# Kernel tuning notes

Hardware: AMD Instinct MI355X
Metric: run time of the kernel (lower is better)

The kernel has to match this reference:

```python
import jax, jax.numpy as jnp
import numpy as np
from jax import lax

DIM = 2048
HEAD_DIM = 128
N_HEADS = 16
N_KV_HEADS = 4
N_REP = N_HEADS // N_KV_HEADS
K_CHUNK = 8          # token_chunk
SEQ = 2048
BATCH = 1
ROPE_THETA = 10000.0
KV_DIM = N_KV_HEADS * HEAD_DIM  # 512


def _make_freq_cis(seq, hd, theta):
    # (seq, hd//2, 2, 2) rotation matrices [[cos, -sin], [sin, cos]]
    inv = 1.0 / (theta ** (np.arange(0, hd, 2, dtype=np.float64) / hd))
    ang = np.outer(np.arange(seq, dtype=np.float64), inv)
    cos, sin = np.cos(ang), np.sin(ang)
    f = np.stack([np.stack([cos, -sin], -1), np.stack([sin, cos], -1)], -2)
    return jnp.asarray(f, jnp.float32)


def setup_inputs() -> dict:
    key = jax.random.key(0)
    ks = jax.random.split(key, 12)
    s = 0.02
    inp = {
        'x': jax.random.normal(ks[0], (BATCH, SEQ, DIM), jnp.float32),
        'freq_cis': _make_freq_cis(SEQ, HEAD_DIM, ROPE_THETA),
        # nn.Linear weights stored as (out, in); y = x @ W.T
        'wq': jax.random.normal(ks[1], (N_HEADS * HEAD_DIM, DIM), jnp.float32) * s,
        'wk': jax.random.normal(ks[2], (KV_DIM, DIM), jnp.float32) * s,
        'wv': jax.random.normal(ks[3], (KV_DIM, DIM), jnp.float32) * s,
        'wo': jax.random.normal(ks[4], (DIM, N_HEADS * HEAD_DIM), jnp.float32) * s,
        # diagonal SSM params for k_ssm / v_ssm (per-channel)
        'a_log_k': jax.random.normal(ks[5], (KV_DIM,), jnp.float32) * 0.5,
        'b_k': jax.random.normal(ks[6], (KV_DIM,), jnp.float32),
        'c_k': jax.random.normal(ks[7], (KV_DIM,), jnp.float32),
        'a_log_v': jax.random.normal(ks[8], (KV_DIM,), jnp.float32) * 0.5,
        'b_v': jax.random.normal(ks[9], (KV_DIM,), jnp.float32),
        'c_v': jax.random.normal(ks[10], (KV_DIM,), jnp.float32),
    }
    return inp


def _ssm_chunked(x, a_log, b, c):
    # Chunked diagonal SSM with state reset every K_CHUNK tokens
    # (equivalent to flat_process_chunks_with_ssm with boundaries every K).
    bsz, S, E = x.shape
    nc = S // K_CHUNK
    a = jnp.exp(-jax.nn.softplus(a_log))  # (E,) decay in (0, 1)
    xs = x.reshape(bsz * nc, K_CHUNK, E).swapaxes(0, 1)  # (K, N, E)

    def step(h, xt):
        h = a * h + b * xt
        return h, c * h

    _, ys = lax.scan(step, jnp.zeros((bsz * nc, E), x.dtype), xs)
    return ys.swapaxes(0, 1).reshape(bsz, S, E)


def _apply_rope(xq, xk, freq_cis):
    # xq: (b, s, h, hd); freq_cis: (s, hd//2, 2, 2)
    def rot(t):
        b, s, h, hd = t.shape
        tr = t.reshape(b, s, h, hd // 2, 1, 2)
        f = freq_cis.reshape(1, s, 1, hd // 2, 2, 2)
        return (tr * f).sum(-1).reshape(b, s, h, hd)
    return rot(xq), rot(xk)


def _forward(x, freq_cis, wq, wk, wv, wo, a_log_k, b_k, c_k, a_log_v, b_v, c_v):
    bsz, S, _ = x.shape
    xq = jnp.einsum('bsd,ed->bse', x, wq)
    xk = jnp.einsum('bsd,ed->bse', x, wk)
    xv = jnp.einsum('bsd,ed->bse', x, wv)

    # chunked SSM preprocessing of K/V (+ residual_ssm)
    xk_p = _ssm_chunked(xk, a_log_k, b_k, c_k) + xk
    xv_p = _ssm_chunked(xv, a_log_v, b_v, c_v) + xv

    xq = xq.reshape(bsz, S, N_HEADS, HEAD_DIM)
    xk_p = xk_p.reshape(bsz, S, N_KV_HEADS, HEAD_DIM)
    xv_p = xv_p.reshape(bsz, S, N_KV_HEADS, HEAD_DIM)

    xq, xk_p = _apply_rope(xq, xk_p, freq_cis)

    # GQA repeat_kv (torch.repeat_interleave on head dim)
    xk_p = jnp.repeat(xk_p, N_REP, axis=2)
    xv_p = jnp.repeat(xv_p, N_REP, axis=2)

    # chunk-boundary attention mask
    k_pos = jnp.arange(S)
    boundary = (k_pos % K_CHUNK) == (K_CHUNK - 1)
    t = jnp.arange(S)[:, None]
    k = k_pos[None, :]
    mask = ((k < t) & boundary[None, :]) | (k == t - 1) | ((k < 4) & (k <= t))

    q = xq.transpose(0, 2, 1, 3)   # (b, h, s, d)
    kk = xk_p.transpose(0, 2, 1, 3)
    vv = xv_p.transpose(0, 2, 1, 3)

    scores = jnp.einsum('bhqd,bhkd->bhqk', q, kk) / jnp.sqrt(
        jnp.asarray(HEAD_DIM, q.dtype))
    scores = jnp.where(mask[None, None], scores, -jnp.inf)
    attn = jax.nn.softmax(scores, axis=-1)
    out = jnp.einsum('bhqk,bhkd->bhqd', attn, vv)
    out = out.transpose(0, 2, 1, 3).reshape(bsz, S, N_HEADS * HEAD_DIM)
    return jnp.einsum('bse,de->bsd', out, wo)


def reference(x, freq_cis, wq, wk, wv, wo, a_log_k, b_k, c_k,
              a_log_v, b_v, c_v):
    return _forward(x, freq_cis, wq, wk, wv, wo,
                    a_log_k, b_k, c_k, a_log_v, b_v, c_v)
```

## Files before the change

kernel.cpp:

```cpp
#include <hip/hip_runtime.h>

typedef __bf16 bf16x8 __attribute__((ext_vector_type(8)));
typedef float  f32x4  __attribute__((ext_vector_type(4)));
typedef unsigned short u16;
typedef unsigned int   u32;

__device__ __forceinline__ float b2f(u16 u) {
    u32 x = ((u32)u) << 16;
    return __builtin_bit_cast(float, x);
}
__device__ __forceinline__ u16 f2b(float f) {
    u32 x = __builtin_bit_cast(u32, f);
    x += 0x7fffu + ((x >> 16) & 1u);
    return (u16)(x >> 16);
}

__global__ void convert_kernel(const float* __restrict__ x, const float* __restrict__ wq,
                               const float* __restrict__ wk, const float* __restrict__ wv,
                               const float* __restrict__ wo,
                               u16* __restrict__ xb, u16* __restrict__ wcat, u16* __restrict__ wob)
{
    long i4 = (long)blockIdx.x * 256 + threadIdx.x;
    long e = i4 * 4;
    const float* src; u16* dst;
    if (e < 4194304) { src = x + e; dst = xb + e; }
    else if (e < 10485760) {
        long j = e - 4194304;
        dst = wcat + j;
        if (j < 4194304)      src = wq + j;
        else if (j < 5242880) src = wk + (j - 4194304);
        else                  src = wv + (j - 5242880);
    } else {
        long j = e - 10485760;
        src = wo + j; dst = wob + j;
    }
    float4 v = *(const float4*)src;
    uint2 pk;
    pk.x = (u32)f2b(v.x) | ((u32)f2b(v.y) << 16);
    pk.y = (u32)f2b(v.z) | ((u32)f2b(v.w) << 16);
    *(uint2*)dst = pk;
}

template<int MODE>
__global__ __launch_bounds__(256) void gemm_bt_kernel(
    const u16* __restrict__ A, const u16* __restrict__ B,
    void* __restrict__ Cout, int M, int N, int K,
    u16* __restrict__ qb, u16* __restrict__ c1kv, const float* __restrict__ fc)
{
    __shared__ u16 As[2][8192];
    __shared__ u16 Bs[2][4096];
    const int tid  = threadIdx.x;
    const int lane = tid & 63;
    const int wave = tid >> 6;
    const int waveM = wave >> 1, waveN = wave & 1;
    const int tm = blockIdx.y * 128;
    const int tn = blockIdx.x * 64;

    f32x4 acc[4][2];
#pragma unroll
    for (int i = 0; i < 4; ++i)
#pragma unroll
        for (int j = 0; j < 2; ++j) acc[i][j] = f32x4{0.f, 0.f, 0.f, 0.f};

    const int frow = lane & 15;
    const int fk   = (lane >> 4) * 8;

    auto STAGE = [&](int buf, int kt) {
#pragma unroll
        for (int c = 0; c < 4; ++c) {
            int idx = c * 256 + tid;
            int row = idx >> 3;
            int blk = (idx & 7) ^ (row & 7);
            const u16* srcA = A + (size_t)(tm + row) * K + kt + blk * 8;
            u16* dstA = &As[buf][(size_t)(c * 256 + wave * 64) * 8];
            __builtin_amdgcn_global_load_lds((const __attribute__((address_space(1))) void*)srcA,
                                             (__attribute__((address_space(3))) void*)dstA, 16, 0, 0);
        }
#pragma unroll
        for (int c = 0; c < 2; ++c) {
            int idx = c * 256 + tid;
            int row = idx >> 3;
            int blk = (idx & 7) ^ (row & 7);
            const u16* srcB = B + (size_t)(tn + row) * K + kt + blk * 8;
            u16* dstB = &Bs[buf][(size_t)(c * 256 + wave * 64) * 8];
            __builtin_amdgcn_global_load_lds((const __attribute__((address_space(1))) void*)srcB,
                                             (__attribute__((address_space(3))) void*)dstB, 16, 0, 0);
        }
    };
    auto COMPUTE = [&](int buf) {
#pragma unroll
        for (int kk = 0; kk < 64; kk += 32) {
            bf16x8 af[4], bfr[2];
#pragma unroll
            for (int m = 0; m < 4; ++m) {
                int r  = waveM * 64 + m * 16 + frow;
                int kb_ = ((kk + fk) >> 3) ^ (r & 7);
                af[m] = *(const bf16x8*)&As[buf][r * 64 + kb_ * 8];
            }
#pragma unroll
            for (int n = 0; n < 2; ++n) {
                int r  = waveN * 32 + n * 16 + frow;
                int kb_ = ((kk + fk) >> 3) ^ (r & 7);
                bfr[n] = *(const bf16x8*)&Bs[buf][r * 64 + kb_ * 8];
            }
#pragma unroll
            for (int m = 0; m < 4; ++m)
#pragma unroll
                for (int n = 0; n < 2; ++n)
                    acc[m][n] = __builtin_amdgcn_mfma_f32_16x16x32_bf16(af[m], bfr[n], acc[m][n], 0, 0, 0);
        }
    };

    const int nk = K >> 6;
    STAGE(0, 0);
    int buf = 0;
    for (int t = 0; t < nk - 1; ++t) {
        STAGE(buf ^ 1, (t + 1) << 6);
        asm volatile("s_waitcnt vmcnt(6)" ::: "memory");
        __builtin_amdgcn_s_barrier();
        __builtin_amdgcn_sched_barrier(0);
        COMPUTE(buf);
        __builtin_amdgcn_sched_barrier(0);
        __builtin_amdgcn_s_barrier();
        buf ^= 1;
    }
    asm volatile("s_waitcnt vmcnt(0)" ::: "memory");
    __builtin_amdgcn_s_barrier();
    __builtin_amdgcn_sched_barrier(0);
    COMPUTE(buf);

    const int rb = tm + waveM * 64;
    const int cb = tn + waveN * 32;
    const int s  = lane & 15;
    if (MODE == 0) {
#pragma unroll
        for (int m = 0; m < 4; ++m)
#pragma unroll
            for (int n = 0; n < 2; ++n)
#pragma unroll
                for (int r = 0; r < 4; ++r) {
                    int row = rb + m * 16 + (lane >> 4) * 4 + r;
                    int col = cb + n * 16 + s;
                    ((float*)Cout)[(size_t)row * N + col] = acc[m][n][r];
                }
    } else if (tn < 2048) {
#pragma unroll
        for (int m = 0; m < 4; ++m)
#pragma unroll
            for (int n = 0; n < 2; ++n)
#pragma unroll
                for (int r = 0; r < 4; ++r) {
                    int row = rb + m * 16 + (lane >> 4) * 4 + r;
                    int col = cb + n * 16 + s;
                    float val  = acc[m][n][r];
                    float part = __shfl_xor(val, 1);
                    int i = (col & 127) >> 1;
                    const float* f4 = &fc[((size_t)row * 64 + i) * 4];
                    float cs = f4[0], sn = f4[2];
                    float q = (s & 1) ? (part * sn + val * cs)
                                      : (val * cs - part * sn);
                    qb[(size_t)row * 2048 + col] = f2b(q);
                }
    } else {
#pragma unroll
        for (int m = 0; m < 4; ++m)
#pragma unroll
            for (int n = 0; n < 2; ++n)
#pragma unroll
                for (int r = 0; r < 4; ++r) {
                    int row = rb + m * 16 + (lane >> 4) * 4 + r;
                    int col = cb + n * 16 + s;
                    c1kv[(size_t)row * 1024 + (col - 2048)] = f2b(acc[m][n][r]);
                }
    }
}

__global__ void ssm_kv_kernel(const u16* __restrict__ c1kv, const float* __restrict__ fc,
                              const float* __restrict__ alk, const float* __restrict__ bk,
                              const float* __restrict__ ck,
                              const float* __restrict__ alv, const float* __restrict__ bv,
                              const float* __restrict__ cv,
                              u16* __restrict__ kb, u16* __restrict__ vb,
                              u16* __restrict__ kbc, u16* __restrict__ vbt)
{
    int gi = blockIdx.x * 256 + threadIdx.x;
    if (gi < 65536) {
        int chunk = gi >> 8, pr = gi & 255;
        int i = pr & 63;
        int e0 = (pr >> 6) * 128 + 2 * i;
        float z0 = alk[e0], z1 = alk[e0 + 1];
        float sp0 = z0 > 20.f ? z0 : log1pf(__expf(z0));
        float sp1 = z1 > 20.f ? z1 : log1pf(__expf(z1));
        float a0 = __expf(-sp0), a1 = __expf(-sp1);
        float b0 = bk[e0], b1 = bk[e0 + 1];
        float c0 = ck[e0], cc1 = ck[e0 + 1];
        float h0 = 0.f, h1 = 0.f;
        int kvh = e0 >> 7, d = e0 & 127;
#pragma unroll
        for (int tt = 0; tt < 8; ++tt) {
            int sr = chunk * 8 + tt;
            u32 u = *(const u32*)&c1kv[(size_t)sr * 1024 + e0];
            float x0 = b2f((u16)(u & 0xffff)), x1 = b2f((u16)(u >> 16));
            h0 = a0 * h0 + b0 * x0;
            h1 = a1 * h1 + b1 * x1;
            float y0 = c0 * h0 + x0;
            float y1 = cc1 * h1 + x1;
            const float* f4 = &fc[((size_t)sr * 64 + i) * 4];
            float k0 = y0 * f4[0] - y1 * f4[2];
            float k1 = y0 * f4[2] + y1 * f4[0];
            u32 pk = (u32)f2b(k0) | ((u32)f2b(k1) << 16);
            *(u32*)&kb[(size_t)sr * 512 + e0] = pk;
            if (tt == 7)
                *(u32*)&kbc[(size_t)kvh * 32768 + chunk * 128 + d] = pk;
        }
    } else {
        int vi = gi - 65536;
        int chunk = vi >> 9, e = vi & 511;
        float z = alv[e];
        float sp = z > 20.f ? z : log1pf(__expf(z));
        float a = __expf(-sp);
        float b = bv[e], c = cv[e];
        float h = 0.f;
#pragma unroll
        for (int tt = 0; tt < 8; ++tt) {
            int sr = chunk * 8 + tt;
            float xvv = b2f(c1kv[(size_t)sr * 1024 + 512 + e]);
            h = a * h + b * xvv;
            u16 y = f2b(c * h + xvv);
            vb[(size_t)sr * 512 + e] = y;
            if (tt == 7)
                vbt[((size_t)e << 8) + chunk] = y;
        }
    }
}

__global__ __launch_bounds__(512, 2) void attn_kernel(
    const u16* __restrict__ qb, const u16* __restrict__ kb, const u16* __restrict__ vb,
    const u16* __restrict__ kbc, const u16* __restrict__ vbt, u16* __restrict__ aout)
{
    __shared__ u16   ksbuf[32768];
    __shared__ u16   vsbuf[32768];
    __shared__ float p_ext[8][16][32];

    const int tid  = threadIdx.x;
    const int w    = tid >> 6;
    const int lane = tid & 63;
    const int s    = lane & 15;
    const int g    = lane >> 4;
    const int h    = blockIdx.x >> 4;
    const int t0   = (blockIdx.x & 15) * 128;
    const int kvh  = h >> 2;
    const int qw   = t0 + w * 16;

    {
        const u16* kcb = kbc + ((size_t)kvh << 15);
#pragma unroll
        for (int it = 0; it < 8; ++it) {
            int idx = it * 512 + tid;
            int r = idx >> 4, b = idx & 15;
            const u16* src = kcb + r * 128 + ((b ^ (r & 7)) << 3);
            u16* dst = ksbuf + (size_t)(it * 512 + w * 64) * 8;
            __builtin_amdgcn_global_load_lds((const __attribute__((address_space(1))) void*)src,
                                             (__attribute__((address_space(3))) void*)dst, 16, 0, 0);
        }
    }
    __syncthreads();

    {
        const u16* vtb = vbt + ((size_t)kvh << 15);
#pragma unroll
        for (int it = 0; it < 8; ++it) {
            int idx = it * 512 + tid;
            int r = idx >> 5, b = idx & 31;
            const u16* src = vtb + r * 256 + ((b ^ (r & 7)) << 3);
            u16* dst = vsbuf + (size_t)(it * 512 + w * 64) * 8;
            __builtin_amdgcn_global_load_lds((const __attribute__((address_space(1))) void*)src,
                                             (__attribute__((address_space(3))) void*)dst, 16, 0, 0);
        }
    }

    bf16x8 qa[4];
    {
        const u16* qr = qb + (size_t)(qw + s) * 2048 + h * 128 + g * 8;
#pragma unroll
        for (int kk = 0; kk < 4; ++kk) qa[kk] = *(const bf16x8*)&qr[kk * 32];
    }

    f32x4 sf[18];
#pragma unroll
    for (int i = 0; i < 18; ++i) sf[i] = f32x4{0.f, 0.f, 0.f, 0.f};

#pragma unroll
    for (int fb = 0; fb < 16; ++fb) {
        int row = fb * 16 + s;
#pragma unroll
        for (int kk = 0; kk < 4; ++kk) {
            int ch = (kk * 4 + g) ^ (s & 7);
            bf16x8 bf = *(const bf16x8*)&ksbuf[row * 128 + ch * 8];
            sf[fb] = __builtin_amdgcn_mfma_f32_16x16x32_bf16(qa[kk], bf, sf[fb], 0, 0, 0);
        }
    }
#pragma unroll
    for (int xb = 0; xb < 2; ++xb) {
        int i = xb * 16 + s;
        int keyrow = (i < 4) ? i : (qw + (i - 4) - 1);
        if (keyrow < 0) keyrow = 0;
        if (keyrow > 2047) keyrow = 2047;
        const u16* kr = kb + (size_t)keyrow * 512 + kvh * 128 + g * 8;
#pragma unroll
        for (int kk = 0; kk < 4; ++kk) {
            bf16x8 bf = *(const bf16x8*)&kr[kk * 32];
            sf[16 + xb] = __builtin_amdgcn_mfma_f32_16x16x32_bf16(qa[kk], bf, sf[16 + xb], 0, 0, 0);
        }
    }

    const float scale = 0.08838834764831845f;
    float mx[4] = {-1e30f, -1e30f, -1e30f, -1e30f};
#pragma unroll
    for (int fi = 0; fi < 18; ++fi)
#pragma unroll
        for (int r = 0; r < 4; ++r) {
            int q = g * 4 + r;
            int t = qw + q;
            bool ok;
            if (fi < 16) {
                int j = fi * 16 + s;
                ok = j < (t >> 3);
            } else {
                int i = (fi - 16) * 16 + s;
                if (i < 4) ok = (i <= t);
                else       ok = ((i - 4) == q) && ((t & 7) != 0) && (t >= 5);
            }
            float v = ok ? sf[fi][r] * scale : -1e30f;
            sf[fi][r] = v;
            mx[r] = fmaxf(mx[r], v);
        }
#pragma unroll
    for (int r = 0; r < 4; ++r)
#pragma unroll
        for (int off = 8; off; off >>= 1) mx[r] = fmaxf(mx[r], __shfl_xor(mx[r], off));

    float sm[4] = {0.f, 0.f, 0.f, 0.f};
#pragma unroll
    for (int fi = 0; fi < 18; ++fi)
#pragma unroll
        for (int r = 0; r < 4; ++r) {
            float p = __expf(sf[fi][r] - mx[r]);
            sf[fi][r] = p;
            sm[r] += p;
        }
#pragma unroll
    for (int r = 0; r < 4; ++r)
#pragma unroll
        for (int off = 8; off; off >>= 1) sm[r] += __shfl_xor(sm[r], off);
    float inv[4];
#pragma unroll
    for (int r = 0; r < 4; ++r) inv[r] = 1.f / sm[r];

    __syncthreads();

    u16* pbuf = ksbuf + w * 4096;
#pragma unroll
    for (int fi = 0; fi < 16; ++fi)
#pragma unroll
        for (int r = 0; r < 4; ++r) {
            int q = g * 4 + r;
            int c = fi * 16 + s;
            int blk = (c >> 3) ^ q;
            pbuf[q * 256 + (blk << 3) + (c & 7)] = f2b(sf[fi][r]);
        }
#pragma unroll
    for (int xb = 0; xb < 2; ++xb)
#pragma unroll
        for (int r = 0; r < 4; ++r)
            p_ext[w][g * 4 + r][xb * 16 + s] = sf[16 + xb][r];

    bf16x8 pa[8];
#pragma unroll
    for (int kk = 0; kk < 8; ++kk) {
        int blk = (kk * 4 + g) ^ s;
        pa[kk] = *(const bf16x8*)&pbuf[s * 256 + (blk << 3)];
    }
    f32x4 out[8];
#pragma unroll
    for (int f = 0; f < 8; ++f) out[f] = f32x4{0.f, 0.f, 0.f, 0.f};
#pragma unroll
    for (int f = 0; f < 8; ++f) {
        int row = f * 16 + s;
#pragma unroll
        for (int kk = 0; kk < 8; ++kk) {
            int ch = (kk * 4 + g) ^ (s & 7);
            bf16x8 vf = *(const bf16x8*)&vsbuf[row * 256 + ch * 8];
            out[f] = __builtin_amdgcn_mfma_f32_16x16x32_bf16(pa[kk], vf, out[f], 0, 0, 0);
        }
    }

    {
        float v4[4][8];
#pragma unroll
        for (int e = 0; e < 4; ++e)
#pragma unroll
            for (int f = 0; f < 8; ++f)
                v4[e][f] = b2f(vb[(size_t)e * 512 + kvh * 128 + f * 16 + s]);
#pragma unroll
        for (int r = 0; r < 4; ++r) {
            int q = g * 4 + r;
            int t = qw + q;
#pragma unroll
            for (int e = 0; e < 4; ++e) {
                float p = p_ext[w][q][e];
#pragma unroll
                for (int f = 0; f < 8; ++f) out[f][r] += p * v4[e][f];
            }
            float pp = p_ext[w][q][4 + q];
            int key = t - 1; if (key < 0) key = 0;
            const u16* vr = vb + (size_t)key * 512 + kvh * 128;
#pragma unroll
            for (int f = 0; f < 8; ++f) out[f][r] += pp * b2f(vr[f * 16 + s]);
        }
    }

#pragma unroll
    for (int f = 0; f < 8; ++f)
#pragma unroll
        for (int r = 0; r < 4; ++r) {
            int t = qw + g * 4 + r;
            aout[(size_t)t * 2048 + h * 128 + f * 16 + s] = f2b(out[f][r] * inv[r]);
        }
}

extern "C" void kernel_launch(void* const* d_in, const int* in_sizes, int n_in,
                              void* d_out, int out_size, void* d_ws, size_t ws_size,
                              hipStream_t stream) {
    const float* x   = (const float*)d_in[0];
    const float* fc  = (const float*)d_in[1];
    const float* wq  = (const float*)d_in[2];
    const float* wk  = (const float*)d_in[3];
    const float* wv  = (const float*)d_in[4];
    const float* wo  = (const float*)d_in[5];
    const float* alk = (const float*)d_in[6];
    const float* bk  = (const float*)d_in[7];
    const float* ck  = (const float*)d_in[8];
    const float* alv = (const float*)d_in[9];
    const float* bv  = (const float*)d_in[10];
    const float* cv  = (const float*)d_in[11];

    char* ws = (char*)d_ws;
    u16*   xb   = (u16*)(ws);
    u16*   wcat = (u16*)(ws + 8388608);
    u16*   wob  = (u16*)(ws + 20971520);
    u16*   c1kv = (u16*)(ws + 29360128);
    u16*   qb   = (u16*)(ws + 54525952);
    u16*   kb   = (u16*)(ws + 62914560);
    u16*   vb   = (u16*)(ws + 65011712);
    u16*   kbc  = (u16*)(ws + 67108864);
    u16*   vbt  = (u16*)(ws + 67371008);
    u16*   aout = (u16*)(ws + 67633152);

    convert_kernel<<<14336, 256, 0, stream>>>(x, wq, wk, wv, wo, xb, wcat, wob);

    dim3 g1(3072 / 64, 2048 / 128);
    gemm_bt_kernel<1><<<g1, 256, 0, stream>>>(xb, wcat, nullptr, 2048, 3072, 2048,
                                              qb, c1kv, fc);

    ssm_kv_kernel<<<768, 256, 0, stream>>>(c1kv, fc, alk, bk, ck, alv, bv, cv,
                                           kb, vb, kbc, vbt);

    attn_kernel<<<256, 512, 0, stream>>>(qb, kb, vb, kbc, vbt, aout);

    dim3 g3(2048 / 64, 2048 / 128);
    gemm_bt_kernel<0><<<g3, 256, 0, stream>>>(aout, wob, d_out, 2048, 2048, 2048,
                                              nullptr, nullptr, nullptr);
}
```

Baseline: 102.4 us.

## Load GEMM B fragments directly to registers and triple-buffer A tiles

The GEMM no longer stages the B operand through shared memory. Each wave loads its B fragments straight from global memory into registers, double-buffered across iterations. A tiles now use a three-deep LDS ring with one barrier per k-step, so copies for the next tiles overlap compute. This cuts LDS traffic and barrier pressure, but raises register use and makes each wave issue uncoalesced, redundant global reads of B. It also assumes nk is even.

```diff
diff --git a/kernel.cpp b/kernel.cpp
--- a/kernel.cpp
+++ b/kernel.cpp
@@ -47,8 +47,7 @@
     void* __restrict__ Cout, int M, int N, int K,
     u16* __restrict__ qb, u16* __restrict__ c1kv, const float* __restrict__ fc)
 {
-    __shared__ u16 As[2][8192];
-    __shared__ u16 Bs[2][4096];
+    __shared__ u16 As[3][8192];
     const int tid  = threadIdx.x;
     const int lane = tid & 63;
     const int wave = tid >> 6;
@@ -64,74 +63,88 @@
 
     const int frow = lane & 15;
     const int fk   = (lane >> 4) * 8;
-
-    auto STAGE = [&](int buf, int kt) {
+    const size_t Ksz = (size_t)K;
+
+    const u16* Bbase = B + (size_t)(tn + waveN * 32 + frow) * Ksz + fk;
+
+    auto STAGE_A = [&](int buf, int kt) {
 #pragma unroll
         for (int c = 0; c < 4; ++c) {
             int idx = c * 256 + tid;
             int row = idx >> 3;
             int blk = (idx & 7) ^ (row & 7);
-            const u16* srcA = A + (size_t)(tm + row) * K + kt + blk * 8;
+            const u16* srcA = A + (size_t)(tm + row) * Ksz + kt + blk * 8;
             u16* dstA = &As[buf][(size_t)(c * 256 + wave * 64) * 8];
             __builtin_amdgcn_global_load_lds((const __attribute__((address_space(1))) void*)srcA,
                                              (__attribute__((address_space(3))) void*)dstA, 16, 0, 0);
         }
-#pragma unroll
-        for (int c = 0; c < 2; ++c) {
-            int idx = c * 256 + tid;
-            int row = idx >> 3;
-            int blk = (idx & 7) ^ (row & 7);
-            const u16* srcB = B + (size_t)(tn + row) * K + kt + blk * 8;
-            u16* dstB = &Bs[buf][(size_t)(c * 256 + wave * 64) * 8];
-            __builtin_amdgcn_global_load_lds((const __attribute__((address_space(1))) void*)srcB,
-                                             (__attribute__((address_space(3))) void*)dstB, 16, 0, 0);
-        }
     };
-    auto COMPUTE = [&](int buf) {
-#pragma unroll
-        for (int kk = 0; kk < 64; kk += 32) {
-            bf16x8 af[4], bfr[2];
-#pragma unroll
-            for (int m = 0; m < 4; ++m) {
-                int r  = waveM * 64 + m * 16 + frow;
-                int kb_ = ((kk + fk) >> 3) ^ (r & 7);
-                af[m] = *(const bf16x8*)&As[buf][r * 64 + kb_ * 8];
-            }
-#pragma unroll
-            for (int n = 0; n < 2; ++n) {
-                int r  = waveN * 32 + n * 16 + frow;
-                int kb_ = ((kk + fk) >> 3) ^ (r & 7);
-                bfr[n] = *(const bf16x8*)&Bs[buf][r * 64 + kb_ * 8];
-            }
-#pragma unroll
-            for (int m = 0; m < 4; ++m)
-#pragma unroll
-                for (int n = 0; n < 2; ++n)
-                    acc[m][n] = __builtin_amdgcn_mfma_f32_16x16x32_bf16(af[m], bfr[n], acc[m][n], 0, 0, 0);
-        }
-    };
+
+#define LOADB(dst, kt_) {                                          \
+        dst[0] = *(const bf16x8*)&Bbase[(kt_)];                    \
+        dst[1] = *(const bf16x8*)&Bbase[16 * Ksz + (kt_)];         \
+        dst[2] = *(const bf16x8*)&Bbase[(kt_) + 32];               \
+        dst[3] = *(const bf16x8*)&Bbase[16 * Ksz + (kt_) + 32]; }
+
+#define COMPUTE(bufi, bp) {                                        \
+        _Pragma("unroll")                                          \
+        for (int kk2 = 0; kk2 < 2; ++kk2) {                        \
+            bf16x8 af[4];                                          \
+            _Pragma("unroll")                                      \
+            for (int m = 0; m < 4; ++m) {                          \
+                int r  = waveM * 64 + m * 16 + frow;               \
+                int kb_ = ((kk2 * 32 + fk) >> 3) ^ (r & 7);        \
+                af[m] = *(const bf16x8*)&As[bufi][r * 64 + kb_ * 8]; \
+            }                                                      \
+            _Pragma("unroll")                                      \
+            for (int m = 0; m < 4; ++m)                            \
+                _Pragma("unroll")                                  \
+                for (int n = 0; n < 2; ++n)                        \
+                    acc[m][n] = __builtin_amdgcn_mfma_f32_16x16x32_bf16( \
+                        af[m], bp[kk2 * 2 + n], acc[m][n], 0, 0, 0); \
+        } }
 
     const int nk = K >> 6;
-    STAGE(0, 0);
-    int buf = 0;
-    for (int t = 0; t < nk - 1; ++t) {
-        STAGE(buf ^ 1, (t + 1) << 6);
-        asm volatile("s_waitcnt vmcnt(6)" ::: "memory");
+    bf16x8 bA[4], bB[4];
+
+    STAGE_A(0, 0);
+    STAGE_A(1, 64);
+    LOADB(bA, 0);
+
+    int ra = 0, rb = 1, rc = 2;
+    for (int t = 0; t < nk - 2; t += 2) {
+        LOADB(bB, (t + 1) << 6);
+        __builtin_amdgcn_sched_barrier(0);
+        asm volatile("s_waitcnt vmcnt(8)" ::: "memory");
         __builtin_amdgcn_s_barrier();
         __builtin_amdgcn_sched_barrier(0);
-        COMPUTE(buf);
+        STAGE_A(rc, (t + 2) << 6);
+        COMPUTE(ra, bA);
+        LOADB(bA, (t + 2) << 6);
         __builtin_amdgcn_sched_barrier(0);
+        asm volatile("s_waitcnt vmcnt(8)" ::: "memory");
         __builtin_amdgcn_s_barrier();
-        buf ^= 1;
-    }
+        __builtin_amdgcn_sched_barrier(0);
+        STAGE_A(ra, (t + 3) << 6);
+        COMPUTE(rb, bB);
+        int tmp = rc; rc = rb; rb = ra; ra = tmp;
+    }
+    LOADB(bB, (nk - 1) << 6);
+    __builtin_amdgcn_sched_barrier(0);
+    asm volatile("s_waitcnt vmcnt(8)" ::: "memory");
+    __builtin_amdgcn_s_barrier();
+    __builtin_amdgcn_sched_barrier(0);
+    COMPUTE(ra, bA);
     asm volatile("s_waitcnt vmcnt(0)" ::: "memory");
     __builtin_amdgcn_s_barrier();
     __builtin_amdgcn_sched_barrier(0);
-    COMPUTE(buf);
-
-    const int rb = tm + waveM * 64;
-    const int cb = tn + waveN * 32;
-    const int s  = lane & 15;
+    COMPUTE(rb, bB);
+#undef LOADB
+#undef COMPUTE
+
+    const int rbr = tm + waveM * 64;
+    const int cb  = tn + waveN * 32;
+    const int s   = lane & 15;
     if (MODE == 0) {
 #pragma unroll
         for (int m = 0; m < 4; ++m)
@@ -139,7 +152,7 @@
             for (int n = 0; n < 2; ++n)
 #pragma unroll
                 for (int r = 0; r < 4; ++r) {
-                    int row = rb + m * 16 + (lane >> 4) * 4 + r;
+                    int row = rbr + m * 16 + (lane >> 4) * 4 + r;
                     int col = cb + n * 16 + s;
                     ((float*)Cout)[(size_t)row * N + col] = acc[m][n][r];
                 }
@@ -150,7 +163,7 @@
             for (int n = 0; n < 2; ++n)
 #pragma unroll
                 for (int r = 0; r < 4; ++r) {
-                    int row = rb + m * 16 + (lane >> 4) * 4 + r;
+                    int row = rbr + m * 16 + (lane >> 4) * 4 + r;
                     int col = cb + n * 16 + s;
                     float val  = acc[m][n][r];
                     float part = __shfl_xor(val, 1);
@@ -168,7 +181,7 @@
             for (int n = 0; n < 2; ++n)
 #pragma unroll
                 for (int r = 0; r < 4; ++r) {
-                    int row = rb + m * 16 + (lane >> 4) * 4 + r;
+                    int row = rbr + m * 16 + (lane >> 4) * 4 + r;
                     int col = cb + n * 16 + s;
                     c1kv[(size_t)row * 1024 + (col - 2048)] = f2b(acc[m][n][r]);
                 }
```

Result: slower. 141.3 us (+37.9%).
